# Optimization experiments

Measured on AMD Instinct MI355X. Metric: run time of the kernel, lower is better.

Reference implementation:

```python
import jax, jax.numpy as jnp
import numpy as np

TOP_K = 2          # routed top_k = top_k - num_shared_experts = 3 - 1
CAP_FACTOR = 1.1   # capacity_factor


def setup_inputs() -> dict:
    key = jax.random.key(0)
    ks = jax.random.split(key, 12)
    B, S, D, E = 4, 2048, 1024, 7
    s = 0.02
    return {
        "x": jax.random.normal(ks[0], (B, S, D), jnp.float32),
        "noise": jax.random.normal(ks[1], (B, S, E), jnp.float32),
        "Wr": jax.random.normal(ks[2], (D, E)) * s, "br": jnp.zeros((E,)),
        "Wn": jax.random.normal(ks[3], (D, E)) * s, "bn": jnp.zeros((E,)),
        "W1": jax.random.normal(ks[4], (E, D, D)) * s, "b1": jnp.zeros((E, D)),
        "W2": jax.random.normal(ks[5], (E, D, D)) * s, "b2": jnp.zeros((E, D)),
        "Ws1": jax.random.normal(ks[6], (D, D)) * s, "bs1": jnp.zeros((D,)),
        "Ws2": jax.random.normal(ks[7], (D, D)) * s, "bs2": jnp.zeros((D,)),
    }


def reference(x, noise, Wr, br, Wn, bn, W1, b1, W2, b2, Ws1, bs1, Ws2, bs2):
    B, S, D = x.shape
    E = Wr.shape[1]
    N = B * S
    C = int(N * TOP_K / E * CAP_FACTOR)  # per-expert capacity (static)

    # shared expert (Dropout inactive at inference)
    x_shared = jax.nn.relu(x @ Ws1 + bs1) @ Ws2 + bs2

    # --- noisy top-k router ---
    logits = x @ Wr + br
    noisy = logits + noise * jax.nn.softplus(x @ Wn + bn)
    vals, idx = jax.lax.top_k(noisy, TOP_K)                    # [B,S,K]
    onehot = jax.nn.one_hot(idx, E, dtype=x.dtype)             # [B,S,K,E]
    probs_k = jax.nn.softmax(vals, axis=-1)                    # softmax over -inf-masked logits == softmax over top-k vals
    router_probs = jnp.einsum('bske,bsk->bse', onehot, probs_k)
    expert_mask = onehot.sum(-2)
    lbl = E * (router_probs.mean((0, 1)) * expert_mask.mean((0, 1))).sum()

    # --- capacity-limited dispatch, first-come-first-served in flat token order ---
    flat_x = x.reshape(N, D)
    flat_g = router_probs.reshape(N, E)
    m = (expert_mask.reshape(N, E) > 0).T                      # [E,N] token->expert assignment
    pos = jnp.cumsum(m.astype(jnp.int32), axis=1) - 1          # slot within expert
    valid = m & (pos < C)
    token = jnp.arange(N, dtype=jnp.int32)
    dest = jnp.where(valid, jnp.arange(E, dtype=jnp.int32)[:, None] * C + pos, E * C)
    idxs = jnp.full((E * C + 1,), N, dtype=jnp.int32)
    idxs = idxs.at[dest.reshape(-1)].set(jnp.broadcast_to(token, (E, N)).reshape(-1))
    idxs = idxs[:E * C].reshape(E, C)                          # token id per slot, N = padding

    xpad = jnp.concatenate([flat_x, jnp.zeros((1, D), x.dtype)], axis=0)
    gpad = jnp.concatenate([flat_g, jnp.zeros((1, E), x.dtype)], axis=0)
    xe = xpad[idxs]                                            # [E,C,D]
    h = jax.nn.relu(jnp.einsum('ecd,edh->ech', xe, W1) + b1[:, None, :])
    out = jnp.einsum('ech,ehd->ecd', h, W2) + b2[:, None, :]
    g = (gpad[idxs] * jnp.eye(E, dtype=x.dtype)[:, None, :]).sum(-1)  # [E,C] gate per slot
    slot_valid = (idxs < N).astype(x.dtype)
    weighted = out * (g * slot_valid)[..., None]

    upd = jnp.zeros((N + 1, D), x.dtype).at[idxs.reshape(-1)].add(weighted.reshape(-1, D))[:N]
    final = upd.reshape(B, S, D) + x_shared
    return final, lbl
```

## Files before the change

kernel.cpp:

```cpp
#include <hip/hip_runtime.h>
#include <math.h>

typedef unsigned short u16;
typedef __attribute__((ext_vector_type(4))) float f32x4;
typedef __bf16 bf16x8 __attribute__((ext_vector_type(8)));

#define NTOK 8192
#define DDIM 1024
#define NEXP 7
#define CAPC 2574
#define CPAD 2688
#define EBLK 1176
#define TBLK 1688
#define XCHK 211

__device__ inline float bf2f(u16 u) {
    union { unsigned int i; float f; } c; c.i = ((unsigned int)u) << 16; return c.f;
}
__device__ inline u16 f2bf(float f) {
    union { float f; unsigned int i; } c; c.f = f;
    unsigned int u = c.i;
    unsigned int r = (u + 0x7fffu + ((u >> 16) & 1u)) >> 16;
    return (u16)r;
}

__device__ inline void gl2lds16(const u16* g, const u16* l) {
    __builtin_amdgcn_global_load_lds(
        (const __attribute__((address_space(1))) unsigned int*)g,
        (__attribute__((address_space(3))) unsigned int*)l, 16, 0, 0);
}

__global__ void k_zero(float* out, long n) {
    long i = (long)blockIdx.x * 256 + threadIdx.x;
    long stride = (long)gridDim.x * 256;
    for (; i < n; i += stride) out[i] = 0.f;
}

__device__ inline void tile_transpose(const float* __restrict__ src, u16* __restrict__ dst,
                                      int k0, int n0, int tid, u16 (*tbuf)[256]) {
#pragma unroll
    for (int p = 0; p < 16; ++p) {
        int kl = p * 16 + (tid >> 4);
        int nl = (tid & 15) * 4;
        float4 v = *(const float4*)(src + (long)(k0 + kl) * 1024 + n0 + nl);
        int s = (tid & 7) << 3;
        int kx = kl ^ s;
        tbuf[nl + 0][kx] = f2bf(v.x);
        tbuf[nl + 1][kx] = f2bf(v.y);
        tbuf[nl + 2][kx] = f2bf(v.z);
        tbuf[nl + 3][kx] = f2bf(v.w);
    }
    __syncthreads();
#pragma unroll
    for (int q = 0; q < 8; ++q) {
        int nl = q * 8 + (tid >> 5);
        int kl = (tid & 31) * 8;
        int s = ((nl >> 2) & 7) << 3;
        const u16* pr = &tbuf[nl][kl ^ s];
        ushort4 a = *(const ushort4*)pr;
        ushort4 b = *(const ushort4*)(pr + 4);
        u16* pd = dst + (long)(n0 + nl) * 1024 + k0 + kl;
        *(ushort4*)pd = a;
        *(ushort4*)(pd + 4) = b;
    }
}

__global__ void k_transpose(const float* __restrict__ srcE, const float* __restrict__ srcS,
                            u16* __restrict__ Wt, u16* __restrict__ Wst) {
    __shared__ u16 tbuf[64][256];
    int bid = blockIdx.x, tid = threadIdx.x;
    int z = bid >> 6;
    int rem = bid & 63;
    int k0 = (rem >> 4) * 256;
    int n0 = (rem & 15) * 64;
    const float* src; u16* dst;
    if (z < 7) { src = srcE + (long)z * 1048576; dst = Wt + (long)z * 1048576; }
    else       { src = srcS;                     dst = Wst; }
    tile_transpose(src, dst, k0, n0, tid, tbuf);
}

__global__ __launch_bounds__(512) void k_front(
    const float* __restrict__ x,
    const float* __restrict__ Wr, const float* __restrict__ Wn,
    const float* __restrict__ br, const float* __restrict__ bn,
    const float* __restrict__ noise,
    u16* __restrict__ xb,
    int* __restrict__ idx0, int* __restrict__ idx1,
    float* __restrict__ p0, float* __restrict__ p1,
    int* __restrict__ cnt8, double* __restrict__ sum8,
    int* __restrict__ slot_token, u16* __restrict__ zrow,
    const float* __restrict__ W1, const float* __restrict__ Ws1,
    u16* __restrict__ Wt, u16* __restrict__ Wst,
    const float* __restrict__ W2, const float* __restrict__ Ws2,
    u16* __restrict__ Wt2, u16* __restrict__ Wst2, int ntb) {
    __shared__ union USM {
        struct { float swr[7168]; float swn[7168]; } r;
        u16 tb[64][256];
    } sm;
    __shared__ int sb0[8], sb1[8];
    __shared__ double sq0[8], sq1[8];
    int bid = blockIdx.x, tid = threadIdx.x;

    if (bid >= 1024) {
        int tbk = bid - 1024;
        if (tbk >= ntb) {
            int gid = (tbk - ntb) * 512 + tid;
            if (gid < NEXP * CPAD) slot_token[gid] = NTOK;
            if (gid < DDIM) zrow[gid] = 0;
            return;
        }
        int set = tbk >> 9;
        int t9 = tbk & 511;
        int z = t9 >> 6;
        int rem = t9 & 63;
        int k0 = (rem >> 4) * 256;
        int n0 = (rem & 15) * 64;
        const float* srcE = set ? W2 : W1;
        const float* srcS = set ? Ws2 : Ws1;
        u16* dE = set ? Wt2 : Wt;
        u16* dS = set ? Wst2 : Wst;
        const float* src; u16* dst;
        if (z < 7) { src = srcE + (long)z * 1048576; dst = dE + (long)z * 1048576; }
        else       { src = srcS;                     dst = dS; }
#pragma unroll
        for (int p = 0; p < 8; ++p) {
            int kl = p * 32 + (tid >> 4);
            int nl = (tid & 15) * 4;
            float4 v = *(const float4*)(src + (long)(k0 + kl) * 1024 + n0 + nl);
            int s = (tid & 7) << 3;
            int kx = kl ^ s;
            sm.tb[nl + 0][kx] = f2bf(v.x);
            sm.tb[nl + 1][kx] = f2bf(v.y);
            sm.tb[nl + 2][kx] = f2bf(v.z);
            sm.tb[nl + 3][kx] = f2bf(v.w);
        }
        __syncthreads();
#pragma unroll
        for (int q = 0; q < 4; ++q) {
            int nl = q * 16 + (tid >> 5);
            int kl = (tid & 31) * 8;
            int s = ((nl >> 2) & 7) << 3;
            const u16* pr = &sm.tb[nl][kl ^ s];
            ushort4 a = *(const ushort4*)pr;
            ushort4 b = *(const ushort4*)(pr + 4);
            u16* pd = dst + (long)(n0 + nl) * 1024 + k0 + kl;
            *(ushort4*)pd = a;
            *(ushort4*)(pd + 4) = b;
        }
        return;
    }

    for (int i = tid; i < 7168; i += 512) { sm.r.swr[i] = Wr[i]; sm.r.swn[i] = Wn[i]; }
    __syncthreads();
    int lane = tid & 63, wv = tid >> 6;
    int t = bid * 8 + wv;
    double ar[7] = {0,0,0,0,0,0,0}, an[7] = {0,0,0,0,0,0,0};
    for (int j = 0; j < 16; ++j) {
        int d = j * 64 + lane;
        float xv = x[(long)t * 1024 + d];
        xb[(long)t * 1024 + d] = f2bf(xv);
        double xd = (double)xv;
#pragma unroll
        for (int e = 0; e < 7; ++e) {
            ar[e] += xd * (double)sm.r.swr[d * 7 + e];
            an[e] += xd * (double)sm.r.swn[d * 7 + e];
        }
    }
#pragma unroll
    for (int e = 0; e < 7; ++e) {
        for (int o = 32; o > 0; o >>= 1) {
            ar[e] += __shfl_xor(ar[e], o);
            an[e] += __shfl_xor(an[e], o);
        }
    }
    if (lane == 0) {
        double best = -1e300, second = -1e300; int b0 = 0, b1 = 0;
#pragma unroll
        for (int e = 0; e < 7; ++e) {
            double lg = ar[e] + (double)br[e];
            double z  = an[e] + (double)bn[e];
            double sp = (z > 30.0) ? (z + log1p(exp(-z))) : log1p(exp(z));
            double v  = lg + (double)noise[t * 7 + e] * sp;
            if (v > best)        { second = best; b1 = b0; best = v; b0 = e; }
            else if (v > second) { second = v; b1 = e; }
        }
        double ex = exp(second - best);
        double q0 = 1.0 / (1.0 + ex);
        double q1 = ex / (1.0 + ex);
        idx0[t] = b0; idx1[t] = b1; p0[t] = (float)q0; p1[t] = (float)q1;
        sb0[wv] = b0; sb1[wv] = b1; sq0[wv] = q0; sq1[wv] = q1;
    }
    __syncthreads();
    if (tid < 7) {
        int c = 0; double s = 0.0;
#pragma unroll
        for (int w = 0; w < 8; ++w) {
            if (sb0[w] == tid) { c++; s += sq0[w]; }
            if (sb1[w] == tid) { c++; s += sq1[w]; }
        }
        cnt8[tid * 1024 + bid] = c;
        sum8[tid * 1024 + bid] = s;
    }
}

__global__ __launch_bounds__(1024) void k_scanassign(
    const int* __restrict__ cnt8, const double* __restrict__ sum8,
    const int* __restrict__ idx0, const int* __restrict__ idx1,
    int* __restrict__ slot_token, int* __restrict__ ts0, int* __restrict__ ts1,
    int* __restrict__ cnt, float* __restrict__ out) {
    __shared__ int s[7][128];
    __shared__ int b8[7][1024];
    __shared__ double rd[7][128];
    __shared__ int rawc[7];
    int tid = threadIdx.x, bid = blockIdx.x;
    int e = tid >> 7, i = tid & 127;
    bool act = (e < 7);
    int c8[8]; int v = 0;
    if (act) {
#pragma unroll
        for (int j = 0; j < 8; ++j) { c8[j] = cnt8[e * 1024 + i * 8 + j]; v += c8[j]; }
        s[e][i] = v;
        if (bid == 0) {
            double s64 = 0.0;
#pragma unroll
            for (int j = 0; j < 8; ++j) s64 += sum8[e * 1024 + i * 8 + j];
            rd[e][i] = s64;
        }
    }
    __syncthreads();
    for (int o = 1; o < 128; o <<= 1) {
        int add = (act && i >= o) ? s[e][i - o] : 0;
        __syncthreads();
        if (act) s[e][i] += add;
        __syncthreads();
    }
    if (act) {
        int run = s[e][i] - v;
#pragma unroll
        for (int j = 0; j < 8; ++j) { b8[e][i * 8 + j] = run; run += c8[j]; }
        if (i == 127) {
            rawc[e] = s[e][127];
            if (bid == 0) cnt[e] = (s[e][127] < CAPC) ? s[e][127] : CAPC;
        }
    }
    for (int o = 64; o > 0; o >>= 1) {
        if (bid == 0 && act && i < o) rd[e][i] += rd[e][i + o];
        __syncthreads();
    }
    if (bid == 0 && tid == 0) {
        double acc = 0.0;
        for (int ee = 0; ee < 7; ++ee) acc += rd[ee][0] * (double)rawc[ee];
        out[(long)NTOK * DDIM] = (float)(7.0 * acc / (8192.0 * 8192.0));
    }
    __syncthreads();
    int t = bid * 1024 + tid;
    int lane = tid & 63;
    int i0 = idx0[t], i1 = idx1[t];
    int myts0 = -1, myts1 = -1;
    unsigned long long gm = 0xFFull << ((lane >> 3) * 8);
    unsigned long long lt = (1ull << lane) - 1ull;
    int chunk = t >> 3;
#pragma unroll
    for (int ee = 0; ee < 7; ++ee) {
        bool has = (i0 == ee) || (i1 == ee);
        unsigned long long m = __ballot(has);
        int pre = __popcll(m & lt & gm);
        int pos = b8[ee][chunk] + pre;
        if (has && pos < CAPC) {
            int slot = ee * CPAD + pos;
            slot_token[slot] = t;
            if (i0 == ee) myts0 = slot; else myts1 = slot;
        }
    }
    ts0[t] = myts0; ts1[t] = myts1;
}

template <bool GATHER, bool MODE_H>
__global__ __launch_bounds__(256) void k_gemm(
    const u16* __restrict__ AbaseE, const u16* __restrict__ AbaseS,
    const int* __restrict__ gidx, const u16* __restrict__ zrow,
    const u16* __restrict__ WtE, const u16* __restrict__ WtS,
    const float* __restrict__ biasE, const float* __restrict__ biasS,
    u16* __restrict__ outE, u16* __restrict__ outS,
    const int* __restrict__ cnt) {
    __shared__ __align__(16) u16 ldsA[128 * 64];
    __shared__ __align__(16) u16 ldsB[128 * 64];
    int phys = blockIdx.x;
    int bid = (phys & 7) * XCHK + (phys >> 3);
    int tid = threadIdx.x, lane = tid & 63, wv = tid >> 6;
    int lrow = lane >> 3, lkg = lane & 7;
    int kgs = lkg ^ lrow;

    int e = 0, my, nx;
    const u16* Ab; const u16* Bb; const float* bias; u16* outp;
    bool gather = false;
    if (bid < EBLK) {
        e = bid / 168; int r = bid % 168; my = r >> 3; nx = r & 7;
        if (my * 128 >= cnt[e]) return;
        Ab = AbaseE + (GATHER ? 0L : (long)e * CPAD * 1024);
        Bb = WtE + ((long)e << 20);
        bias = biasE + e * 1024;
        outp = outE + (long)e * CPAD * 1024;
        gather = GATHER;
    } else {
        int sb = bid - EBLK; my = sb >> 3; nx = sb & 7;
        Ab = AbaseS; Bb = WtS; bias = biasS; outp = outS;
    }
    int m0 = my * 128, n0 = nx * 128;

    const u16* arow[4];
    const u16* brow[4];
#pragma unroll
    for (int i = 0; i < 4; ++i) {
        int r = (wv * 4 + i) * 8 + lrow;
        if (gather) {
            int tok = gidx[e * CPAD + m0 + r];
            arow[i] = (tok < NTOK) ? (AbaseE + (long)tok * DDIM) : zrow;
        } else {
            arow[i] = Ab + (long)(m0 + r) * DDIM;
        }
        brow[i] = Bb + (long)(n0 + r) * DDIM;
    }
    f32x4 acc[4][4];
#pragma unroll
    for (int a = 0; a < 4; ++a)
#pragma unroll
        for (int b = 0; b < 4; ++b) { f32x4 z = {0.f, 0.f, 0.f, 0.f}; acc[a][b] = z; }

    int wm = (wv >> 1) * 64, wn = (wv & 1) * 64;
    int rl = lane & 15, quad = lane >> 4;

    for (int k0 = 0; k0 < 1024; k0 += 64) {
#pragma unroll
        for (int i = 0; i < 4; ++i) {
            gl2lds16(arow[i] + k0 + kgs * 8, &ldsA[(wv * 4 + i) * 512]);
            gl2lds16(brow[i] + k0 + kgs * 8, &ldsB[(wv * 4 + i) * 512]);
        }
        __syncthreads();
#pragma unroll
        for (int ks = 0; ks < 2; ++ks) {
            int kg = ks * 4 + quad;
            bf16x8 af[4], bf[4];
#pragma unroll
            for (int mi = 0; mi < 4; ++mi) {
                int row = wm + mi * 16 + rl;
                af[mi] = *(const bf16x8*)&ldsA[row * 64 + (kg ^ (row & 7)) * 8];
            }
#pragma unroll
            for (int ni = 0; ni < 4; ++ni) {
                int row = wn + ni * 16 + rl;
                bf[ni] = *(const bf16x8*)&ldsB[row * 64 + (kg ^ (row & 7)) * 8];
            }
#pragma unroll
            for (int mi = 0; mi < 4; ++mi)
#pragma unroll
                for (int ni = 0; ni < 4; ++ni)
                    acc[mi][ni] = __builtin_amdgcn_mfma_f32_16x16x32_bf16(
                        af[mi], bf[ni], acc[mi][ni], 0, 0, 0);
        }
        __syncthreads();
    }
#pragma unroll
    for (int ni = 0; ni < 4; ++ni) {
        int col = n0 + wn + ni * 16 + rl;
        float bv = bias[col];
#pragma unroll
        for (int mi = 0; mi < 4; ++mi) {
            int rowb = m0 + wm + mi * 16 + quad * 4;
#pragma unroll
            for (int r = 0; r < 4; ++r) {
                float v = acc[mi][ni][r] + bv;
                if constexpr (MODE_H) v = v > 0.f ? v : 0.f;
                outp[(long)(rowb + r) * DDIM + col] = f2bf(v);
            }
        }
    }
}

__global__ __launch_bounds__(256) void k_combine(
    const u16* __restrict__ Xs, const u16* __restrict__ OutE,
    const int* __restrict__ ts0, const int* __restrict__ ts1,
    const float* __restrict__ p0, const float* __restrict__ p1,
    float* __restrict__ out) {
    int b = blockIdx.x;
    int d = threadIdx.x * 4;
    long base = (long)b * DDIM + d;
    ushort4 xs4 = *(const ushort4*)(Xs + base);
    float r0 = bf2f(xs4.x), r1 = bf2f(xs4.y), r2 = bf2f(xs4.z), r3 = bf2f(xs4.w);
    int s0 = ts0[b], s1 = ts1[b];
    if (s0 >= 0) {
        float g = p0[b];
        ushort4 o4 = *(const ushort4*)(OutE + (long)s0 * DDIM + d);
        r0 += g * bf2f(o4.x); r1 += g * bf2f(o4.y); r2 += g * bf2f(o4.z); r3 += g * bf2f(o4.w);
    }
    if (s1 >= 0) {
        float g = p1[b];
        ushort4 o4 = *(const ushort4*)(OutE + (long)s1 * DDIM + d);
        r0 += g * bf2f(o4.x); r1 += g * bf2f(o4.y); r2 += g * bf2f(o4.z); r3 += g * bf2f(o4.w);
    }
    float4 w; w.x = r0; w.y = r1; w.z = r2; w.w = r3;
    *(float4*)(out + base) = w;
}

extern "C" void kernel_launch(void* const* d_in, const int* in_sizes, int n_in,
                              void* d_out, int out_size, void* d_ws, size_t ws_size,
                              hipStream_t stream) {
    const float* x    = (const float*)d_in[0];
    const float* noise= (const float*)d_in[1];
    const float* Wr   = (const float*)d_in[2];
    const float* br   = (const float*)d_in[3];
    const float* Wn   = (const float*)d_in[4];
    const float* bn   = (const float*)d_in[5];
    const float* W1   = (const float*)d_in[6];
    const float* b1   = (const float*)d_in[7];
    const float* W2   = (const float*)d_in[8];
    const float* b2   = (const float*)d_in[9];
    const float* Ws1  = (const float*)d_in[10];
    const float* bs1  = (const float*)d_in[11];
    const float* Ws2  = (const float*)d_in[12];
    const float* bs2  = (const float*)d_in[13];
    float* out = (float*)d_out;
    char* ws = (char*)d_ws;

    size_t off = 0;
    auto alloc = [&](size_t bytes) { size_t o = off; off += (bytes + 255) & ~(size_t)255; return o; };
    u16*  Wt   = (u16*)(ws + alloc(7ull * 1048576 * 2));
    u16*  Wst  = (u16*)(ws + alloc(1048576ull * 2));
    u16*  xb   = (u16*)(ws + alloc((size_t)NTOK * 1024 * 2));
    u16*  He   = (u16*)(ws + alloc((size_t)NEXP * CPAD * 1024 * 2));
    u16*  Hs   = (u16*)(ws + alloc((size_t)NTOK * 1024 * 2));
    u16*  OutE = (u16*)(ws + alloc((size_t)NEXP * CPAD * 1024 * 2));
    u16*  Xs   = (u16*)(ws + alloc((size_t)NTOK * 1024 * 2));
    int*  idx0 = (int*)(ws + alloc(NTOK * 4));
    int*  idx1 = (int*)(ws + alloc(NTOK * 4));
    float* p0  = (float*)(ws + alloc(NTOK * 4));
    float* p1  = (float*)(ws + alloc(NTOK * 4));
    int*  ts0  = (int*)(ws + alloc(NTOK * 4));
    int*  ts1  = (int*)(ws + alloc(NTOK * 4));
    int*  slot_token = (int*)(ws + alloc(NEXP * CPAD * 4));
    int*  cnt8  = (int*)(ws + alloc(7 * 1024 * 4));
    double* sum8 = (double*)(ws + alloc(7 * 1024 * 8));
    int*  cnt    = (int*)(ws + alloc(8 * 4));
    u16*  zrow   = (u16*)(ws + alloc(1024 * 2));
    size_t base_off = off;
    u16*  Wt2  = (u16*)(ws + alloc(7ull * 1048576 * 2));
    u16*  Wst2 = (u16*)(ws + alloc(1048576ull * 2));

    if (base_off > ws_size) {
        k_zero<<<2048, 256, 0, stream>>>(out, (long)out_size);
        return;
    }
    bool sep = (off <= ws_size);
    if (!sep) { Wt2 = Wt; Wst2 = Wst; }
    int ntb = sep ? 1024 : 512;
    int nib = (NEXP * CPAD + 511) / 512;

    k_front<<<1024 + ntb + nib, 512, 0, stream>>>(
        x, Wr, Wn, br, bn, noise, xb, idx0, idx1, p0, p1, cnt8, sum8,
        slot_token, zrow, W1, Ws1, Wt, Wst, W2, Ws2, Wt2, Wst2, ntb);

    k_scanassign<<<8, 1024, 0, stream>>>(
        cnt8, sum8, idx0, idx1, slot_token, ts0, ts1, cnt, out);

    k_gemm<true, true><<<TBLK, 256, 0, stream>>>(
        xb, xb, slot_token, zrow, Wt, Wst, b1, bs1, He, Hs, cnt);

    if (!sep)
        k_transpose<<<512, 256, 0, stream>>>(W2, Ws2, Wt, Wst);

    k_gemm<false, false><<<TBLK, 256, 0, stream>>>(
        He, Hs, nullptr, zrow, Wt2, Wst2, b2, bs2, OutE, Xs, cnt);

    k_combine<<<NTOK, 256, 0, stream>>>(Xs, OutE, ts0, ts1, p0, p1, out);
    (void)in_sizes; (void)n_in; (void)out_size;
}
```

Baseline: 368.5 us.

## Move W2 transpose into first GEMM launch and process two tokens per router wave

The fp32→bf16 transpose of W2/Ws2 moves out of the front kernel and into extra trailing blocks of the first expert GEMM launch. It can then overlap with the GEMM work and fill idle CUs left by early-exiting expert blocks. The router part of the front kernel now has each wave handle two tokens, which halves the router block count and reuses each shared-memory weight load for two accumulations. The cost is more double-precision registers per thread, and the transpose blocks compete with GEMM blocks for CUs.

```diff
diff --git a/kernel.cpp b/kernel.cpp
--- a/kernel.cpp
+++ b/kernel.cpp
@@ -90,38 +90,30 @@
     int* __restrict__ cnt8, double* __restrict__ sum8,
     int* __restrict__ slot_token, u16* __restrict__ zrow,
     const float* __restrict__ W1, const float* __restrict__ Ws1,
-    u16* __restrict__ Wt, u16* __restrict__ Wst,
-    const float* __restrict__ W2, const float* __restrict__ Ws2,
-    u16* __restrict__ Wt2, u16* __restrict__ Wst2, int ntb) {
+    u16* __restrict__ Wt, u16* __restrict__ Wst) {
     __shared__ union USM {
         struct { float swr[7168]; float swn[7168]; } r;
         u16 tb[64][256];
     } sm;
-    __shared__ int sb0[8], sb1[8];
-    __shared__ double sq0[8], sq1[8];
+    __shared__ int sb0[16], sb1[16];
+    __shared__ double sq0[16], sq1[16];
     int bid = blockIdx.x, tid = threadIdx.x;
 
-    if (bid >= 1024) {
-        int tbk = bid - 1024;
-        if (tbk >= ntb) {
-            int gid = (tbk - ntb) * 512 + tid;
+    if (bid >= 512) {
+        int tbk = bid - 512;
+        if (tbk >= 512) {
+            int gid = (tbk - 512) * 512 + tid;
             if (gid < NEXP * CPAD) slot_token[gid] = NTOK;
             if (gid < DDIM) zrow[gid] = 0;
             return;
         }
-        int set = tbk >> 9;
-        int t9 = tbk & 511;
-        int z = t9 >> 6;
-        int rem = t9 & 63;
+        int z = tbk >> 6;
+        int rem = tbk & 63;
         int k0 = (rem >> 4) * 256;
         int n0 = (rem & 15) * 64;
-        const float* srcE = set ? W2 : W1;
-        const float* srcS = set ? Ws2 : Ws1;
-        u16* dE = set ? Wt2 : Wt;
-        u16* dS = set ? Wst2 : Wst;
         const float* src; u16* dst;
-        if (z < 7) { src = srcE + (long)z * 1048576; dst = dE + (long)z * 1048576; }
-        else       { src = srcS;                     dst = dS; }
+        if (z < 7) { src = W1 + (long)z * 1048576; dst = Wt + (long)z * 1048576; }
+        else       { src = Ws1;                    dst = Wst; }
 #pragma unroll
         for (int p = 0; p < 8; ++p) {
             int kl = p * 32 + (tid >> 4);
@@ -153,53 +145,68 @@
     for (int i = tid; i < 7168; i += 512) { sm.r.swr[i] = Wr[i]; sm.r.swn[i] = Wn[i]; }
     __syncthreads();
     int lane = tid & 63, wv = tid >> 6;
-    int t = bid * 8 + wv;
-    double ar[7] = {0,0,0,0,0,0,0}, an[7] = {0,0,0,0,0,0,0};
+    int tA = bid * 16 + wv * 2;
+    int tB = tA + 1;
+    double arA[7] = {0,0,0,0,0,0,0}, anA[7] = {0,0,0,0,0,0,0};
+    double arB[7] = {0,0,0,0,0,0,0}, anB[7] = {0,0,0,0,0,0,0};
     for (int j = 0; j < 16; ++j) {
         int d = j * 64 + lane;
-        float xv = x[(long)t * 1024 + d];
-        xb[(long)t * 1024 + d] = f2bf(xv);
-        double xd = (double)xv;
+        float xvA = x[(long)tA * 1024 + d];
+        float xvB = x[(long)tB * 1024 + d];
+        xb[(long)tA * 1024 + d] = f2bf(xvA);
+        xb[(long)tB * 1024 + d] = f2bf(xvB);
+        double xdA = (double)xvA, xdB = (double)xvB;
 #pragma unroll
         for (int e = 0; e < 7; ++e) {
-            ar[e] += xd * (double)sm.r.swr[d * 7 + e];
-            an[e] += xd * (double)sm.r.swn[d * 7 + e];
+            double wr = (double)sm.r.swr[d * 7 + e];
+            double wn = (double)sm.r.swn[d * 7 + e];
+            arA[e] += xdA * wr; anA[e] += xdA * wn;
+            arB[e] += xdB * wr; anB[e] += xdB * wn;
         }
     }
 #pragma unroll
     for (int e = 0; e < 7; ++e) {
         for (int o = 32; o > 0; o >>= 1) {
-            ar[e] += __shfl_xor(ar[e], o);
-            an[e] += __shfl_xor(an[e], o);
+            arA[e] += __shfl_xor(arA[e], o);
+            anA[e] += __shfl_xor(anA[e], o);
+            arB[e] += __shfl_xor(arB[e], o);
+            anB[e] += __shfl_xor(anB[e], o);
         }
     }
     if (lane == 0) {
-        double best = -1e300, second = -1e300; int b0 = 0, b1 = 0;
-#pragma unroll
-        for (int e = 0; e < 7; ++e) {
-            double lg = ar[e] + (double)br[e];
-            double z  = an[e] + (double)bn[e];
-            double sp = (z > 30.0) ? (z + log1p(exp(-z))) : log1p(exp(z));
-            double v  = lg + (double)noise[t * 7 + e] * sp;
-            if (v > best)        { second = best; b1 = b0; best = v; b0 = e; }
-            else if (v > second) { second = v; b1 = e; }
-        }
-        double ex = exp(second - best);
-        double q0 = 1.0 / (1.0 + ex);
-        double q1 = ex / (1.0 + ex);
-        idx0[t] = b0; idx1[t] = b1; p0[t] = (float)q0; p1[t] = (float)q1;
-        sb0[wv] = b0; sb1[wv] = b1; sq0[wv] = q0; sq1[wv] = q1;
+#pragma unroll
+        for (int h = 0; h < 2; ++h) {
+            int t = h ? tB : tA;
+            double best = -1e300, second = -1e300; int b0 = 0, b1 = 0;
+#pragma unroll
+            for (int e = 0; e < 7; ++e) {
+                double lg = (h ? arB[e] : arA[e]) + (double)br[e];
+                double z  = (h ? anB[e] : anA[e]) + (double)bn[e];
+                double sp = (z > 30.0) ? (z + log1p(exp(-z))) : log1p(exp(z));
+                double v  = lg + (double)noise[t * 7 + e] * sp;
+                if (v > best)        { second = best; b1 = b0; best = v; b0 = e; }
+                else if (v > second) { second = v; b1 = e; }
+            }
+            double ex = exp(second - best);
+            double q0 = 1.0 / (1.0 + ex);
+            double q1 = ex / (1.0 + ex);
+            idx0[t] = b0; idx1[t] = b1; p0[t] = (float)q0; p1[t] = (float)q1;
+            int sl = wv * 2 + h;
+            sb0[sl] = b0; sb1[sl] = b1; sq0[sl] = q0; sq1[sl] = q1;
+        }
     }
     __syncthreads();
-    if (tid < 7) {
+    if (tid < 14) {
+        int e = tid % 7, half = tid / 7;
         int c = 0; double s = 0.0;
 #pragma unroll
         for (int w = 0; w < 8; ++w) {
-            if (sb0[w] == tid) { c++; s += sq0[w]; }
-            if (sb1[w] == tid) { c++; s += sq1[w]; }
-        }
-        cnt8[tid * 1024 + bid] = c;
-        sum8[tid * 1024 + bid] = s;
+            int sl = half * 8 + w;
+            if (sb0[sl] == e) { c++; s += sq0[sl]; }
+            if (sb1[sl] == e) { c++; s += sq1[sl]; }
+        }
+        cnt8[e * 1024 + bid * 2 + half] = c;
+        sum8[e * 1024 + bid * 2 + half] = s;
     }
 }
 
@@ -282,10 +289,23 @@
     const u16* __restrict__ WtE, const u16* __restrict__ WtS,
     const float* __restrict__ biasE, const float* __restrict__ biasS,
     u16* __restrict__ outE, u16* __restrict__ outS,
-    const int* __restrict__ cnt) {
-    __shared__ __align__(16) u16 ldsA[128 * 64];
-    __shared__ __align__(16) u16 ldsB[128 * 64];
+    const int* __restrict__ cnt,
+    const float* __restrict__ trE, const float* __restrict__ trS,
+    u16* __restrict__ trDE, u16* __restrict__ trDS) {
+    __shared__ __align__(16) u16 ldsu[16384];
+    u16* ldsA = ldsu;
+    u16* ldsB = ldsu + 8192;
     int phys = blockIdx.x;
+    if (phys >= TBLK) {
+        int tb = phys - TBLK;
+        int z = tb >> 6, rem = tb & 63;
+        int k0 = (rem >> 4) * 256, n0 = (rem & 15) * 64;
+        const float* src; u16* dst;
+        if (z < 7) { src = trE + (long)z * 1048576; dst = trDE + (long)z * 1048576; }
+        else       { src = trS;                     dst = trDS; }
+        tile_transpose(src, dst, k0, n0, threadIdx.x, (u16(*)[256])ldsu);
+        return;
+    }
     int bid = (phys & 7) * XCHK + (phys >> 3);
     int tid = threadIdx.x, lane = tid & 63, wv = tid >> 6;
     int lrow = lane >> 3, lkg = lane & 7;
@@ -452,24 +472,25 @@
     }
     bool sep = (off <= ws_size);
     if (!sep) { Wt2 = Wt; Wst2 = Wst; }
-    int ntb = sep ? 1024 : 512;
     int nib = (NEXP * CPAD + 511) / 512;
 
-    k_front<<<1024 + ntb + nib, 512, 0, stream>>>(
+    k_front<<<512 + 512 + nib, 512, 0, stream>>>(
         x, Wr, Wn, br, bn, noise, xb, idx0, idx1, p0, p1, cnt8, sum8,
-        slot_token, zrow, W1, Ws1, Wt, Wst, W2, Ws2, Wt2, Wst2, ntb);
+        slot_token, zrow, W1, Ws1, Wt, Wst);
 
     k_scanassign<<<8, 1024, 0, stream>>>(
         cnt8, sum8, idx0, idx1, slot_token, ts0, ts1, cnt, out);
 
-    k_gemm<true, true><<<TBLK, 256, 0, stream>>>(
-        xb, xb, slot_token, zrow, Wt, Wst, b1, bs1, He, Hs, cnt);
+    k_gemm<true, true><<<TBLK + (sep ? 512 : 0), 256, 0, stream>>>(
+        xb, xb, slot_token, zrow, Wt, Wst, b1, bs1, He, Hs, cnt,
+        W2, Ws2, Wt2, Wst2);
 
     if (!sep)
         k_transpose<<<512, 256, 0, stream>>>(W2, Ws2, Wt, Wst);
 
     k_gemm<false, false><<<TBLK, 256, 0, stream>>>(
-        He, Hs, nullptr, zrow, Wt2, Wst2, b2, bs2, OutE, Xs, cnt);
+        He, Hs, nullptr, zrow, Wt2, Wst2, b2, bs2, OutE, Xs, cnt,
+        nullptr, nullptr, nullptr, nullptr);
 
     k_combine<<<NTOK, 256, 0, stream>>>(Xs, OutE, ts0, ts1, p0, p1, out);
     (void)in_sizes; (void)n_in; (void)out_size;
```

Result: slower. 380.0 us (+3.1%).
